# Kernel tuning notes

Measured on AMD Instinct MI355X. Metric: run time of the kernel, lower is better.

Reference implementation:

```python
import jax, jax.numpy as jnp
import numpy as np

NUM_CODE = 8192
CODE_DIM = 256


def setup_inputs() -> dict:
    key = jax.random.key(0)
    k1, k2 = jax.random.split(key)
    z_e = jax.random.normal(k1, (16, CODE_DIM, 32, 32), dtype=jnp.float32)
    span = 1.0 / NUM_CODE
    codebook = jax.random.uniform(k2, (NUM_CODE, CODE_DIM), dtype=jnp.float32,
                                  minval=-span, maxval=span)
    return {"z_e": z_e, "codebook": codebook}


def reference(z_e, codebook):
    # NCHW -> NHWC
    z = jnp.transpose(z_e, (0, 2, 3, 1))  # [B,H,W,D]
    B, H, W, D = z.shape
    flat = z.reshape(-1, D)  # [N,D]
    cb = jax.lax.stop_gradient(codebook)
    # squared L2 distances without materializing [N,K,D] diff tensor
    z2 = jnp.sum(flat * flat, axis=1, keepdims=True)          # [N,1]
    c2 = jnp.sum(cb * cb, axis=1)                              # [K]
    dist = z2 - 2.0 * (flat @ cb.T) + c2[None, :]              # [N,K]
    indices = jnp.argmin(dist, axis=1)                         # [N]
    z_q_flat = cb[indices]                                     # [N,D]
    z_q = z_q_flat.reshape(B, H, W, D)
    # straight-through estimator
    z_q = z + jax.lax.stop_gradient(z_q - z)
    idx = indices.reshape(B, H, W)
    z_q = jnp.transpose(z_q, (0, 3, 1, 2))  # NHWC -> NCHW
    return z_q, idx
```

## Files before the change

kernel.cpp:

```cpp
#include <hip/hip_runtime.h>

typedef __attribute__((ext_vector_type(4))) unsigned int u32x4;
typedef __attribute__((ext_vector_type(4))) int i32x4;

union I16 { u32x4 u; i32x4 i; };

#define SA_INV   (127.0f / 12.0f)
#define SB_INV   (127.0f * 8192.0f)
#define INV_SASB ((127.0 * 127.0 * 8192.0) / 12.0)
#define WI       4500
#define FINF     3.4e38f

__device__ __forceinline__ int q8(float x, float s) {
    int q = (int)__builtin_rintf(x * s);
    return q < -127 ? -127 : (q > 127 ? 127 : q);
}

__global__ void prep_a(const float* __restrict__ z, u32x4* __restrict__ ahi) {
    int o = blockIdx.x * 256 + threadIdx.x;
    int l = o & 63, j = (o >> 6) & 3, rtg = o >> 8;
    int n = rtg * 16 + (l & 15);
    int k0 = j * 64 + ((l >> 4) << 4);
    const float* src = z + ((size_t)(n >> 10) * 256 + k0) * 1024 + (n & 1023);
    u32x4 v;
#pragma unroll
    for (int d = 0; d < 4; ++d) {
        unsigned int w = 0;
#pragma unroll
        for (int b = 0; b < 4; ++b) {
            int q = q8(-2.0f * src[(size_t)(d * 4 + b) * 1024], SA_INV);
            w |= ((unsigned int)(q & 255)) << (8 * b);
        }
        v[d] = w;
    }
    ahi[o] = v;
}

__global__ void prep_b(const float* __restrict__ cb, u32x4* __restrict__ bstr) {
    int o = blockIdx.x * 256 + threadIdx.x;
    int l = o & 63, j = (o >> 6) & 3, ct = o >> 8;
    int code = ct * 16 + (l & 15);
    int k0 = j * 64 + ((l >> 4) << 4);
    const float* src = cb + (size_t)code * 256 + k0;
    u32x4 v;
#pragma unroll
    for (int d = 0; d < 4; ++d) {
        unsigned int w = 0;
#pragma unroll
        for (int b = 0; b < 4; ++b) {
            int q = q8(src[d * 4 + b], SB_INV);
            w |= ((unsigned int)(q & 255)) << (8 * b);
        }
        v[d] = w;
    }
    int stripe = ct >> 5, rr = ct & 31, ch = rr >> 2, t = rr & 3;
    bstr[(size_t)((stripe * 8 + ch) * 1024) + (t * 4 + j) * 64 + l] = v;
}

__global__ void calc_c2(const float* __restrict__ cb, float* __restrict__ c2,
                        unsigned int* __restrict__ ibt) {
    int wid = threadIdx.x >> 6, lane = threadIdx.x & 63;
    int code = blockIdx.x * 4 + wid;
    const float* row = cb + (size_t)code * 256;
    float s = 0.f;
#pragma unroll
    for (int q = 0; q < 4; ++q) { float v = row[q * 64 + lane]; s += v * v; }
#pragma unroll
    for (int m = 32; m >= 1; m >>= 1) s += __shfl_xor(s, m, 64);
    if (lane == 0) {
        c2[code] = s;
        int ib = (int)__builtin_rintf(s * (float)INV_SASB);
        ibt[code] = (((unsigned int)(ib + 262144)) << 6) | (unsigned int)((code >> 4) & 31);
    }
}

__global__ void prep_zt(const float* __restrict__ z, float* __restrict__ zt,
                        float* __restrict__ z2f) {
    __shared__ float tile[32][257];
    int b = blockIdx.x >> 5, h = blockIdx.x & 31;
    int tid = threadIdx.x;
    for (int e = tid; e < 8192; e += 256) {
        int d = e >> 5, w = e & 31;
        tile[w][d] = z[((size_t)(b * 256 + d) * 32 + h) * 32 + w];
    }
    __syncthreads();
    for (int e = tid; e < 8192; e += 256) {
        int w = e >> 8, d = e & 255;
        zt[((size_t)(b * 1024 + h * 32 + w)) * 256 + d] = tile[w][d];
    }
    if (tid < 32) {
        double s = 0.0;
        for (int d = 0; d < 256; ++d) { double v = (double)tile[tid][d]; s += v * v; }
        z2f[b * 1024 + h * 32 + tid] = (float)s;
    }
}

typedef __attribute__((address_space(1))) unsigned int gu32;
typedef __attribute__((address_space(3))) unsigned int lu32;

__global__ __launch_bounds__(256)
void vq_main(const u32x4* __restrict__ ahi4, const u32x4* __restrict__ bstr,
             const unsigned int* __restrict__ ibt,
             unsigned int* __restrict__ cd, int* __restrict__ ci) {
    __shared__ u32x4 lds[2][1024];
    int tid = threadIdx.x;
    int wid = tid >> 6, lane = tid & 63;
    int stripe = blockIdx.x & 15;
    int rg = blockIdx.x >> 4;
    int colc = lane & 15;
    int rt0 = rg * 16 + wid * 4;

    I16 ah[4][4];
#pragma unroll
    for (int rt = 0; rt < 4; ++rt)
#pragma unroll
        for (int j = 0; j < 4; ++j)
            ah[rt][j].u = ahi4[((size_t)(rt0 + rt) * 4 + j) * 64 + lane];

    unsigned int m1[16], m2[16];
#pragma unroll
    for (int s = 0; s < 16; ++s) { m1[s] = 0xFFFFFFFFu; m2[s] = 0xFFFFFFFFu; }

    i32x4 zc = (i32x4){0, 0, 0, 0};

    auto stage = [&](int ch, int buf) {
        const u32x4* g = bstr + (size_t)(stripe * 8 + ch) * 1024 + tid;
        u32x4* d = &lds[buf][0];
#pragma unroll
        for (int it = 0; it < 4; ++it) {
            __builtin_amdgcn_global_load_lds((const gu32*)(g + it * 256),
                                             (lu32*)(d + it * 256 + tid), 16, 0, 0);
        }
    };

    stage(0, 0);
    __syncthreads();

    for (int ch = 0; ch < 8; ++ch) {
        int cur = ch & 1;
        if (ch + 1 < 8) stage(ch + 1, cur ^ 1);

        unsigned int ibtv[4];
#pragma unroll
        for (int t = 0; t < 4; ++t)
            ibtv[t] = ibt[stripe * 512 + ch * 64 + t * 16 + colc];

#pragma unroll
        for (int t = 0; t < 4; ++t) {
            i32x4 acc[4];
            {
                I16 bf; bf.u = lds[cur][(t * 4 + 0) * 64 + lane];
#pragma unroll
                for (int rt = 0; rt < 4; ++rt)
                    acc[rt] = __builtin_amdgcn_mfma_i32_16x16x64_i8(ah[rt][0].i, bf.i, zc, 0, 0, 0);
            }
#pragma unroll
            for (int j = 1; j < 4; ++j) {
                I16 bf; bf.u = lds[cur][(t * 4 + j) * 64 + lane];
#pragma unroll
                for (int rt = 0; rt < 4; ++rt)
                    acc[rt] = __builtin_amdgcn_mfma_i32_16x16x64_i8(ah[rt][j].i, bf.i, acc[rt], 0, 0, 0);
            }
#pragma unroll
            for (int rt = 0; rt < 4; ++rt)
#pragma unroll
                for (int r = 0; r < 4; ++r) {
                    unsigned int key = (((unsigned int)acc[rt][r]) << 6) + ibtv[t];
                    int s = rt * 4 + r;
                    unsigned int disp = m1[s] > key ? m1[s] : key;
                    m1[s] = m1[s] < key ? m1[s] : key;
                    m2[s] = m2[s] < disp ? m2[s] : disp;
                }
        }
        __syncthreads();
    }

#pragma unroll
    for (int s = 0; s < 16; ++s) {
        int rt = s >> 2, r = s & 3;
        int row = (rt0 + rt) * 16 + (lane >> 4) * 4 + r;
        unsigned int v0 = m1[s], v1 = m2[s];
        int c0 = stripe * 512 + (int)(v0 & 63) * 16 + colc;
        int c1 = stripe * 512 + (int)(v1 & 63) * 16 + colc;
        int obase = (row * 16 + stripe) * 3;
#pragma unroll
        for (int k = 0; k < 3; ++k) {
            unsigned int bv; int bi;
            if (v1 < v0) { bv = v1; bi = c1; } else { bv = v0; bi = c0; }
#pragma unroll
            for (int mm = 1; mm < 16; mm <<= 1) {
                unsigned int ov = __shfl_xor(bv, mm, 64);
                int oi = __shfl_xor(bi, mm, 64);
                if (ov < bv || (ov == bv && oi < bi)) { bv = ov; bi = oi; }
            }
            if (colc == k) { cd[obase + k] = bv; ci[obase + k] = bi; }
            if (bi == c0) v0 = 0xFFFFFFFFu;
            if (bi == c1) v1 = 0xFFFFFFFFu;
        }
    }
}

__global__ __launch_bounds__(256)
void refine(const float* __restrict__ zt, const float* __restrict__ z2f,
            const float* __restrict__ cb, const float* __restrict__ c2,
            const unsigned int* __restrict__ cd, const int* __restrict__ ci,
            float* __restrict__ out, int* __restrict__ idxi) {
    int wid = threadIdx.x >> 6, lane = threadIdx.x & 63;
    int n = blockIdx.x * 4 + wid;
    float zq[4];
#pragma unroll
    for (int q = 0; q < 4; ++q) zq[q] = zt[(size_t)n * 256 + q * 64 + lane];
    float z2v = z2f[n];

    unsigned int kd = 0xFFFFFFFFu; int civ = 0;
    if (lane < 48) { kd = cd[n * 48 + lane]; civ = ci[n * 48 + lane]; }
    unsigned int rm = kd;
#pragma unroll
    for (int m = 32; m >= 1; m >>= 1) {
        unsigned int o = __shfl_xor(rm, m, 64);
        rm = o < rm ? o : rm;
    }
    bool active = (lane < 48) && ((kd >> 6) <= (rm >> 6) + WI);
    unsigned long long mask = __ballot(active);
    float bestd = FINF; int besti = 0x7fffffff;
    while (mask) {
        int k = __ffsll(mask) - 1;
        mask &= mask - 1;
        int cidx = __shfl(civ, k, 64);
        const float* crow = cb + (size_t)cidx * 256;
        double dot = 0.0;
#pragma unroll
        for (int q = 0; q < 4; ++q)
            dot += (double)zq[q] * (double)crow[q * 64 + lane];
#pragma unroll
        for (int m = 32; m >= 1; m >>= 1) dot += __shfl_xor(dot, m, 64);
        float Mf = (float)dot;
        float d1 = z2v - 2.0f * Mf;
        float d2 = d1 + c2[cidx];
        if (d2 < bestd || (d2 == bestd && cidx < besti)) { bestd = d2; besti = cidx; }
    }
    if (lane == 0) {
        idxi[n] = besti;
        out[4194304 + n] = (float)besti;
    }
}

__global__ void gather_out(const float* __restrict__ cb,
                           const int* __restrict__ idxi,
                           float* __restrict__ out) {
    __shared__ float tile[32][257];
    __shared__ int sidx[32];
    int b = blockIdx.x >> 5, h = blockIdx.x & 31;
    int tid = threadIdx.x;
    if (tid < 32) sidx[tid] = idxi[(b * 32 + h) * 32 + tid];
    __syncthreads();
    for (int e = tid; e < 8192; e += 256) {
        int w = e >> 8, d = e & 255;
        tile[w][d] = cb[(size_t)sidx[w] * 256 + d];
    }
    __syncthreads();
    for (int e = tid; e < 8192; e += 256) {
        int d = e >> 5, w = e & 31;
        out[(((size_t)b * 256 + d) * 32 + h) * 32 + w] = tile[w][d];
    }
}

extern "C" void kernel_launch(void* const* d_in, const int* in_sizes, int n_in,
                              void* d_out, int out_size, void* d_ws, size_t ws_size,
                              hipStream_t stream) {
    const float* z  = (const float*)d_in[0];
    const float* cb = (const float*)d_in[1];
    float* out = (float*)d_out;
    char* w = (char*)d_ws;
    u32x4* ahi  = (u32x4*)(w);
    u32x4* bstr = (u32x4*)(w + 4194304);
    float* zt   = (float*)(w + 6291456);
    float* c2   = (float*)(w + 23068672);
    unsigned int* ibt = (unsigned int*)(w + 23101440);
    float* z2f  = (float*)(w + 23134208);
    unsigned int* cd = (unsigned int*)(w + 23199744);
    int*   ci   = (int*)(w + 26345472);
    int*   idxi = (int*)(w);

    prep_a<<<1024, 256, 0, stream>>>(z, ahi);
    prep_b<<<512, 256, 0, stream>>>(cb, bstr);
    calc_c2<<<2048, 256, 0, stream>>>(cb, c2, ibt);
    prep_zt<<<512, 256, 0, stream>>>(z, zt, z2f);
    vq_main<<<1024, 256, 0, stream>>>(ahi, bstr, ibt, cd, ci);
    refine<<<4096, 256, 0, stream>>>(zt, z2f, cb, c2, cd, ci, out, idxi);
    gather_out<<<512, 256, 0, stream>>>(cb, idxi, out);
}
```

Before: 188.3 us.

## Fuse prep kernels and double LDS chunk size in int8 VQ main loop

Merges the four preprocessing kernels into two: one kernel per input that transposes, computes squared norms and quantizes to int8 from a shared-memory tile, instead of reading z and the codebook multiple times. The main MFMA kernel now stages 128 codes per chunk (4 chunks instead of 8), halving barriers, fully unrolls the chunk loop and sets launch bounds for 2 blocks per CU. The top-2 min update is rewritten in min/max form. In exchange it uses more LDS and registers, and the z2 partial-sum reduction moves to shared memory.

```diff
diff --git a/kernel.cpp b/kernel.cpp
--- a/kernel.cpp
+++ b/kernel.cpp
@@ -15,69 +15,16 @@
     int q = (int)__builtin_rintf(x * s);
     return q < -127 ? -127 : (q > 127 ? 127 : q);
 }
-
-__global__ void prep_a(const float* __restrict__ z, u32x4* __restrict__ ahi) {
-    int o = blockIdx.x * 256 + threadIdx.x;
-    int l = o & 63, j = (o >> 6) & 3, rtg = o >> 8;
-    int n = rtg * 16 + (l & 15);
-    int k0 = j * 64 + ((l >> 4) << 4);
-    const float* src = z + ((size_t)(n >> 10) * 256 + k0) * 1024 + (n & 1023);
-    u32x4 v;
-#pragma unroll
-    for (int d = 0; d < 4; ++d) {
-        unsigned int w = 0;
-#pragma unroll
-        for (int b = 0; b < 4; ++b) {
-            int q = q8(-2.0f * src[(size_t)(d * 4 + b) * 1024], SA_INV);
-            w |= ((unsigned int)(q & 255)) << (8 * b);
-        }
-        v[d] = w;
-    }
-    ahi[o] = v;
-}
-
-__global__ void prep_b(const float* __restrict__ cb, u32x4* __restrict__ bstr) {
-    int o = blockIdx.x * 256 + threadIdx.x;
-    int l = o & 63, j = (o >> 6) & 3, ct = o >> 8;
-    int code = ct * 16 + (l & 15);
-    int k0 = j * 64 + ((l >> 4) << 4);
-    const float* src = cb + (size_t)code * 256 + k0;
-    u32x4 v;
-#pragma unroll
-    for (int d = 0; d < 4; ++d) {
-        unsigned int w = 0;
-#pragma unroll
-        for (int b = 0; b < 4; ++b) {
-            int q = q8(src[d * 4 + b], SB_INV);
-            w |= ((unsigned int)(q & 255)) << (8 * b);
-        }
-        v[d] = w;
-    }
-    int stripe = ct >> 5, rr = ct & 31, ch = rr >> 2, t = rr & 3;
-    bstr[(size_t)((stripe * 8 + ch) * 1024) + (t * 4 + j) * 64 + l] = v;
-}
-
-__global__ void calc_c2(const float* __restrict__ cb, float* __restrict__ c2,
-                        unsigned int* __restrict__ ibt) {
-    int wid = threadIdx.x >> 6, lane = threadIdx.x & 63;
-    int code = blockIdx.x * 4 + wid;
-    const float* row = cb + (size_t)code * 256;
-    float s = 0.f;
-#pragma unroll
-    for (int q = 0; q < 4; ++q) { float v = row[q * 64 + lane]; s += v * v; }
-#pragma unroll
-    for (int m = 32; m >= 1; m >>= 1) s += __shfl_xor(s, m, 64);
-    if (lane == 0) {
-        c2[code] = s;
-        int ib = (int)__builtin_rintf(s * (float)INV_SASB);
-        ibt[code] = (((unsigned int)(ib + 262144)) << 6) | (unsigned int)((code >> 4) & 31);
-    }
-}
-
-__global__ void prep_zt(const float* __restrict__ z, float* __restrict__ zt,
-                        float* __restrict__ z2f) {
+__device__ __forceinline__ unsigned int umin(unsigned int a, unsigned int b) { return a < b ? a : b; }
+__device__ __forceinline__ unsigned int umax(unsigned int a, unsigned int b) { return a > b ? a : b; }
+
+__global__ __launch_bounds__(256)
+void prep_z(const float* __restrict__ z, u32x4* __restrict__ ahi,
+            float* __restrict__ zt, float* __restrict__ z2f) {
     __shared__ float tile[32][257];
-    int b = blockIdx.x >> 5, h = blockIdx.x & 31;
+    __shared__ double pz[32][9];
+    int bh = blockIdx.x;
+    int b = bh >> 5, h = bh & 31;
     int tid = threadIdx.x;
     for (int e = tid; e < 8192; e += 256) {
         int d = e >> 5, w = e & 31;
@@ -86,23 +33,89 @@
     __syncthreads();
     for (int e = tid; e < 8192; e += 256) {
         int w = e >> 8, d = e & 255;
-        zt[((size_t)(b * 1024 + h * 32 + w)) * 256 + d] = tile[w][d];
-    }
+        zt[(size_t)(bh * 32 + w) * 256 + d] = tile[w][d];
+    }
+    {
+        int w = tid >> 3, seg = tid & 7;
+        double s = 0.0;
+#pragma unroll
+        for (int d = 0; d < 32; ++d) { double v = (double)tile[w][seg * 32 + d]; s += v * v; }
+        pz[w][seg] = s;
+    }
+    __syncthreads();
     if (tid < 32) {
         double s = 0.0;
-        for (int d = 0; d < 256; ++d) { double v = (double)tile[tid][d]; s += v * v; }
-        z2f[b * 1024 + h * 32 + tid] = (float)s;
-    }
+#pragma unroll
+        for (int seg = 0; seg < 8; ++seg) s += pz[tid][seg];
+        z2f[bh * 32 + tid] = (float)s;
+    }
+    for (int o = tid; o < 512; o += 256) {
+        int l = o & 63, j = (o >> 6) & 3, tt = o >> 8;
+        int wp = tt * 16 + (l & 15);
+        int k0 = j * 64 + ((l >> 4) << 4);
+        u32x4 v;
+#pragma unroll
+        for (int d = 0; d < 4; ++d) {
+            unsigned int wv = 0;
+#pragma unroll
+            for (int bb = 0; bb < 4; ++bb) {
+                int q = q8(-2.0f * tile[wp][k0 + d * 4 + bb], SA_INV);
+                wv |= ((unsigned int)(q & 255)) << (8 * bb);
+            }
+            v[d] = wv;
+        }
+        ahi[(size_t)bh * 512 + o] = v;
+    }
+}
+
+__global__ __launch_bounds__(256)
+void prep_cb(const float* __restrict__ cb, float* __restrict__ c2,
+             unsigned int* __restrict__ ibt, u32x4* __restrict__ bstr) {
+    __shared__ float tile[16][257];
+    __shared__ float pc[16][17];
+    int ct = blockIdx.x;
+    int tid = threadIdx.x;
+    int cl = tid >> 4, dseg = tid & 15;
+    const float* src = cb + (size_t)(ct * 16 + cl) * 256 + dseg * 16;
+    float s = 0.f;
+#pragma unroll
+    for (int i = 0; i < 16; ++i) { float v = src[i]; tile[cl][dseg * 16 + i] = v; s += v * v; }
+    pc[cl][dseg] = s;
+    __syncthreads();
+    if (tid < 16) {
+        float t = 0.f;
+#pragma unroll
+        for (int i = 0; i < 16; ++i) t += pc[tid][i];
+        int code = ct * 16 + tid;
+        c2[code] = t;
+        int ib = (int)__builtin_rintf(t * (float)INV_SASB);
+        ibt[code] = (((unsigned int)(ib + 262144)) << 6) | (unsigned int)((code >> 4) & 31);
+    }
+    int l = tid & 63, j = tid >> 6;
+    int code_l = l & 15, k0 = j * 64 + ((l >> 4) << 4);
+    u32x4 v;
+#pragma unroll
+    for (int d = 0; d < 4; ++d) {
+        unsigned int wv = 0;
+#pragma unroll
+        for (int bb = 0; bb < 4; ++bb) {
+            int q = q8(tile[code_l][k0 + d * 4 + bb], SB_INV);
+            wv |= ((unsigned int)(q & 255)) << (8 * bb);
+        }
+        v[d] = wv;
+    }
+    int stripe = ct >> 5, rr = ct & 31, ch = rr >> 3, t_in = rr & 7;
+    bstr[(size_t)(stripe * 4 + ch) * 2048 + (t_in * 4 + j) * 64 + l] = v;
 }
 
 typedef __attribute__((address_space(1))) unsigned int gu32;
 typedef __attribute__((address_space(3))) unsigned int lu32;
 
-__global__ __launch_bounds__(256)
+__global__ __launch_bounds__(256, 2)
 void vq_main(const u32x4* __restrict__ ahi4, const u32x4* __restrict__ bstr,
              const unsigned int* __restrict__ ibt,
              unsigned int* __restrict__ cd, int* __restrict__ ci) {
-    __shared__ u32x4 lds[2][1024];
+    __shared__ u32x4 lds[2][2048];
     int tid = threadIdx.x;
     int wid = tid >> 6, lane = tid & 63;
     int stripe = blockIdx.x & 15;
@@ -124,10 +137,10 @@
     i32x4 zc = (i32x4){0, 0, 0, 0};
 
     auto stage = [&](int ch, int buf) {
-        const u32x4* g = bstr + (size_t)(stripe * 8 + ch) * 1024 + tid;
+        const u32x4* g = bstr + (size_t)(stripe * 4 + ch) * 2048 + tid;
         u32x4* d = &lds[buf][0];
 #pragma unroll
-        for (int it = 0; it < 4; ++it) {
+        for (int it = 0; it < 8; ++it) {
             __builtin_amdgcn_global_load_lds((const gu32*)(g + it * 256),
                                              (lu32*)(d + it * 256 + tid), 16, 0, 0);
         }
@@ -136,17 +149,18 @@
     stage(0, 0);
     __syncthreads();
 
-    for (int ch = 0; ch < 8; ++ch) {
+#pragma unroll
+    for (int ch = 0; ch < 4; ++ch) {
         int cur = ch & 1;
-        if (ch + 1 < 8) stage(ch + 1, cur ^ 1);
-
-        unsigned int ibtv[4];
-#pragma unroll
-        for (int t = 0; t < 4; ++t)
-            ibtv[t] = ibt[stripe * 512 + ch * 64 + t * 16 + colc];
-
-#pragma unroll
-        for (int t = 0; t < 4; ++t) {
+        if (ch < 3) stage(ch + 1, cur ^ 1);
+
+        unsigned int ibtv[8];
+#pragma unroll
+        for (int t = 0; t < 8; ++t)
+            ibtv[t] = ibt[stripe * 512 + ch * 128 + t * 16 + colc];
+
+#pragma unroll
+        for (int t = 0; t < 8; ++t) {
             i32x4 acc[4];
             {
                 I16 bf; bf.u = lds[cur][(t * 4 + 0) * 64 + lane];
@@ -167,9 +181,8 @@
                 for (int r = 0; r < 4; ++r) {
                     unsigned int key = (((unsigned int)acc[rt][r]) << 6) + ibtv[t];
                     int s = rt * 4 + r;
-                    unsigned int disp = m1[s] > key ? m1[s] : key;
-                    m1[s] = m1[s] < key ? m1[s] : key;
-                    m2[s] = m2[s] < disp ? m2[s] : disp;
+                    m2[s] = umin(umax(key, m1[s]), m2[s]);
+                    m1[s] = umin(m1[s], key);
                 }
         }
         __syncthreads();
@@ -282,10 +295,8 @@
     int*   ci   = (int*)(w + 26345472);
     int*   idxi = (int*)(w);
 
-    prep_a<<<1024, 256, 0, stream>>>(z, ahi);
-    prep_b<<<512, 256, 0, stream>>>(cb, bstr);
-    calc_c2<<<2048, 256, 0, stream>>>(cb, c2, ibt);
-    prep_zt<<<512, 256, 0, stream>>>(z, zt, z2f);
+    prep_cb<<<512, 256, 0, stream>>>(cb, c2, ibt, bstr);
+    prep_z<<<512, 256, 0, stream>>>(z, ahi, zt, z2f);
     vq_main<<<1024, 256, 0, stream>>>(ahi, bstr, ibt, cd, ci);
     refine<<<4096, 256, 0, stream>>>(zt, z2f, cb, c2, cd, ci, out, idxi);
     gather_out<<<512, 256, 0, stream>>>(cb, idxi, out);
```

New measurement: 429.6 us. 2.28x slower.
